# Optimization experiments

Hardware: AMD Instinct MI355X
Metric: run time of the kernel (lower is better)

The kernel has to match this reference:

```python
import jax, jax.numpy as jnp
import numpy as np

N_NODES = 50000
N_EDGES = 800000
IN_FEAT = 256
OUT_FEAT = 256
NUM_RELS = 8
ALPHA = 0.5


def setup_inputs() -> dict:
    key = jax.random.key(0)
    k1, k2, k3, k4, k5, k6 = jax.random.split(key, 6)
    x = jax.random.normal(k1, (N_NODES, IN_FEAT), dtype=jnp.float32)
    edge_index = jax.random.randint(k2, (2, N_EDGES), 0, N_NODES, dtype=jnp.int64)
    edge_type = jax.random.randint(k3, (N_EDGES,), 0, NUM_RELS, dtype=jnp.int64)
    # Xavier-uniform-ish init for weights (scale per fan-in/fan-out)
    gain = float(np.sqrt(2.0))  # calculate_gain('relu')
    lim_w = gain * float(np.sqrt(6.0 / (IN_FEAT + OUT_FEAT)))
    weight = jax.random.uniform(k4, (NUM_RELS, IN_FEAT, OUT_FEAT), dtype=jnp.float32,
                                minval=-lim_w, maxval=lim_w)
    loop_weight = jax.random.uniform(k5, (IN_FEAT, OUT_FEAT), dtype=jnp.float32,
                                     minval=-lim_w, maxval=lim_w)
    h_bias = jnp.zeros((OUT_FEAT,), dtype=jnp.float32)
    return {"edge_index": edge_index, "x": x, "edge_type": edge_type,
            "weight": weight, "h_bias": h_bias, "loop_weight": loop_weight}


def reference(edge_index, x, edge_type, weight, h_bias, loop_weight):
    num_nodes = x.shape[0]
    src, dst = edge_index[0], edge_index[1]
    # Per-edge message msg_e = x[src_e] @ weight[edge_type_e].
    # Computed efficiently as num_rels dense GEMMs over all nodes, then a fused
    # (relation, src) gather — identical math, avoids (E, in, out) weight blowup.
    hx = jnp.einsum('ni,rio->rno', x, weight)          # (R, N, out)
    msg = hx[edge_type, src]                            # (E, out)
    agg = jax.ops.segment_sum(msg, dst, num_segments=num_nodes)  # (N, out)
    node_repr = agg * jnp.asarray(ALPHA, x.dtype) ** 0.5
    node_repr = node_repr + h_bias
    loop_message = x @ loop_weight                      # (N, out)
    node_repr = node_repr + loop_message * jnp.asarray(1.0 - ALPHA, x.dtype) ** 0.5
    # activation=None, dropout=0.0 (eval) -> identity
    return node_repr
```

## Files before the change

### kernel.cpp

```cpp
#include <hip/hip_runtime.h>

typedef __bf16 bf16x8 __attribute__((ext_vector_type(8)));
typedef float f32x4 __attribute__((ext_vector_type(4)));

static __device__ __forceinline__ unsigned short f2bf(float f) {
    unsigned u = __builtin_bit_cast(unsigned, f);
    u += 0x7FFFu + ((u >> 16) & 1u);
    return (unsigned short)(u >> 16);
}
static __device__ __forceinline__ float bf2f(unsigned short h) {
    return __builtin_bit_cast(float, ((unsigned)h) << 16);
}

#define GLOAD_LDS16(g, l)                                              \
    __builtin_amdgcn_global_load_lds(                                  \
        (const __attribute__((address_space(1))) unsigned int*)(g),    \
        (__attribute__((address_space(3))) unsigned int*)(l), 16, 0, 0)

__global__ __launch_bounds__(256) void rgcn_zero(unsigned* __restrict__ p, int n) {
    int i = blockIdx.x * 256 + threadIdx.x;
    if (i < n) p[i] = 0;
}

__global__ __launch_bounds__(256) void rgcn_hist(const int* __restrict__ ei,
                                                 unsigned* __restrict__ cnt, int E) {
    int e = blockIdx.x * 256 + threadIdx.x;
    if (e < E) atomicAdd(&cnt[ei[E + e]], 1u);
}

__global__ __launch_bounds__(1024) void rgcn_scan1(const unsigned* __restrict__ cnt,
                                                   unsigned* __restrict__ off,
                                                   unsigned* __restrict__ bsum, int n) {
    __shared__ unsigned ws[16];
    const int t = threadIdx.x, lane = t & 63, wv = t >> 6;
    int i = blockIdx.x * 1024 + t;
    unsigned v = (i < n) ? cnt[i] : 0;
    unsigned s = v;
    #pragma unroll
    for (int d = 1; d < 64; d <<= 1) {
        unsigned u = __shfl_up(s, d, 64);
        if (lane >= d) s += u;
    }
    if (lane == 63) ws[wv] = s;
    __syncthreads();
    if (wv == 0) {
        unsigned b = (lane < 16) ? ws[lane] : 0;
        unsigned sb = b;
        #pragma unroll
        for (int d = 1; d < 16; d <<= 1) {
            unsigned u = __shfl_up(sb, d, 64);
            if (lane >= d) sb += u;
        }
        if (lane < 16) ws[lane] = sb - b;
        if (lane == 15) bsum[blockIdx.x] = sb;
    }
    __syncthreads();
    if (i < n) off[i] = ws[wv] + (s - v);
}

__global__ __launch_bounds__(64) void rgcn_scan2(unsigned* __restrict__ bsum,
                                                 unsigned* __restrict__ bsumo,
                                                 unsigned* __restrict__ off, int nb, int n) {
    const int lane = threadIdx.x & 63;
    unsigned b = (lane < nb) ? bsum[lane] : 0;
    unsigned s = b;
    #pragma unroll
    for (int d = 1; d < 64; d <<= 1) {
        unsigned u = __shfl_up(s, d, 64);
        if (lane >= d) s += u;
    }
    if (lane < nb) bsumo[lane] = s - b;
    if (lane == 63) off[n] = s;
}

__global__ __launch_bounds__(256) void rgcn_scan3(unsigned* __restrict__ off,
                                                  const unsigned* __restrict__ bsumo,
                                                  unsigned* __restrict__ cur, int n) {
    int i = blockIdx.x * 256 + threadIdx.x;
    if (i < n) {
        unsigned v = off[i] + bsumo[i >> 10];
        off[i] = v;
        cur[i] = v;
    }
}

__global__ __launch_bounds__(256) void rgcn_scatter(const int* __restrict__ ei,
                                                    const int* __restrict__ et,
                                                    unsigned* __restrict__ cur,
                                                    unsigned* __restrict__ recs, int E) {
    int e = blockIdx.x * 256 + threadIdx.x;
    if (e < E) {
        int dst = ei[E + e];
        unsigned p = atomicAdd(&cur[dst], 1u);
        recs[p] = (unsigned)ei[e] | ((unsigned)et[e] << 16);
    }
}

__global__ __launch_bounds__(256) void rgcn_cvt(const float* __restrict__ x,
                                                unsigned short* __restrict__ Z, int M) {
    int w = (blockIdx.x * 256 + threadIdx.x) >> 6;
    int lane = threadIdx.x & 63;
    if (w >= M) return;
    float4 v = *(const float4*)(x + (size_t)w * 256 + lane * 4);
    ushort4 o;
    o.x = f2bf(v.x); o.y = f2bf(v.y); o.z = f2bf(v.z); o.w = f2bf(v.w);
    *(ushort4*)(Z + (size_t)w * 2304 + 2048 + lane * 4) = o;
}

__global__ __launch_bounds__(256) void rgcn_wbt(const float* __restrict__ w,
                                                const float* __restrict__ lw,
                                                unsigned short* __restrict__ wbT) {
    int kc = blockIdx.x * 256 + threadIdx.x;
    int n  = blockIdx.y;
    if (kc >= 2304) return;
    float v;
    if (kc < 2048) {
        int r = kc >> 8, k = kc & 255;
        v = w[((size_t)r * 256 + k) * 256 + n];
    } else {
        v = lw[(size_t)(kc - 2048) * 256 + n];
    }
    wbT[(size_t)n * 2304 + kc] = f2bf(v * 0.70710678118654752f);
}

__global__ __launch_bounds__(256) void rgcn_agg(const unsigned* __restrict__ recs,
                                                const unsigned* __restrict__ off,
                                                unsigned short* __restrict__ Z, int M) {
    int w = (blockIdx.x * 256 + threadIdx.x) >> 6;
    int lane = threadIdx.x & 63;
    if (w >= M) return;
    unsigned o0 = off[w], o1 = off[w + 1];
    f32x4 a0 = {}, a1 = {}, a2 = {}, a3 = {}, a4 = {}, a5 = {}, a6 = {}, a7 = {};

#define LOADF(rec, fv)                                                                 \
    {                                                                                  \
        const ushort4 v_ = *(const ushort4*)(Z + (size_t)((rec) & 0xFFFFu) * 2304 +    \
                                             2048 + lane * 4);                         \
        fv[0] = bf2f(v_.x); fv[1] = bf2f(v_.y); fv[2] = bf2f(v_.z); fv[3] = bf2f(v_.w);\
    }
#define ACCUM(rec, fv)                                                                 \
    switch ((rec) >> 16) {                                                             \
        case 0: a0 += fv; break; case 1: a1 += fv; break;                              \
        case 2: a2 += fv; break; case 3: a3 += fv; break;                              \
        case 4: a4 += fv; break; case 5: a5 += fv; break;                              \
        case 6: a6 += fv; break; default: a7 += fv; break;                             \
    }

    unsigned i = o0;
    for (; i + 4 <= o1; i += 4) {
        unsigned r0 = recs[i], r1 = recs[i + 1], r2 = recs[i + 2], r3 = recs[i + 3];
        f32x4 f0, f1, f2, f3;
        LOADF(r0, f0); LOADF(r1, f1); LOADF(r2, f2); LOADF(r3, f3);
        ACCUM(r0, f0); ACCUM(r1, f1); ACCUM(r2, f2); ACCUM(r3, f3);
    }
    for (; i < o1; ++i) {
        unsigned r0 = recs[i];
        f32x4 f0;
        LOADF(r0, f0);
        ACCUM(r0, f0);
    }
#undef LOADF
#undef ACCUM

    unsigned short* zr = Z + (size_t)w * 2304 + lane * 4;
#define ST(rr, ax)                                                                     \
    {                                                                                  \
        ushort4 o_;                                                                    \
        o_.x = f2bf(ax[0]); o_.y = f2bf(ax[1]); o_.z = f2bf(ax[2]); o_.w = f2bf(ax[3]);\
        *(ushort4*)(zr + rr * 256) = o_;                                               \
    }
    ST(0, a0) ST(1, a1) ST(2, a2) ST(3, a3) ST(4, a4) ST(5, a5) ST(6, a6) ST(7, a7)
#undef ST
}

#define BM 128
#define BN 128
#define BK 64

__global__ __launch_bounds__(256) void rgcn_gemm(
    const unsigned short* __restrict__ A,
    const unsigned short* __restrict__ Bt,
    float* __restrict__ out,
    const float* __restrict__ bias,
    int M)
{
    __shared__ char lds[2 * BM * BK * 2];
    char* Ab = lds;
    char* Bb = lds + BM * BK * 2;

    const int tid  = threadIdx.x;
    const int lane = tid & 63;
    const int wid  = tid >> 6;
    const int wm   = (wid >> 1) * 64;
    const int wn   = (wid & 1) * 64;
    const int n0   = blockIdx.x * BN;
    const int m0   = blockIdx.y * BM;

    f32x4 acc[4][4] = {};

    int st_r[4], st_scb[4];
    #pragma unroll
    for (int it = 0; it < 4; ++it) {
        int o = it * 4096 + tid * 16;
        int r = o >> 7;
        st_r[it]   = r;
        st_scb[it] = (o & 127) ^ ((r & 7) << 4);
    }

    for (int kt = 0; kt < 2304; kt += BK) {
        __syncthreads();
        #pragma unroll
        for (int it = 0; it < 4; ++it) {
            const int r = st_r[it], scb = st_scb[it];
            int ga = m0 + r; if (ga >= M) ga = M - 1;
            const char* gA = (const char*)A + (size_t)ga * 4608 + (size_t)kt * 2 + scb;
            GLOAD_LDS16(gA, Ab + it * 4096 + tid * 16);
            const char* gB = (const char*)Bt + (size_t)(n0 + r) * 4608 + (size_t)kt * 2 + scb;
            GLOAD_LDS16(gB, Bb + it * 4096 + tid * 16);
        }
        __syncthreads();
        #pragma unroll
        for (int kk = 0; kk < 2; ++kk) {
            const int koff = kk * 32 + (lane >> 4) * 8;
            bf16x8 af[4], bfr[4];
            #pragma unroll
            for (int i = 0; i < 4; ++i) {
                int ar = wm + i * 16 + (lane & 15);
                af[i] = *(const bf16x8*)(Ab + ((ar * (BK * 2) + koff * 2) ^ ((ar & 7) << 4)));
                int br = wn + i * 16 + (lane & 15);
                bfr[i] = *(const bf16x8*)(Bb + ((br * (BK * 2) + koff * 2) ^ ((br & 7) << 4)));
            }
            #pragma unroll
            for (int i = 0; i < 4; ++i)
                #pragma unroll
                for (int j = 0; j < 4; ++j)
                    acc[i][j] = __builtin_amdgcn_mfma_f32_16x16x32_bf16(af[i], bfr[j], acc[i][j], 0, 0, 0);
        }
    }

    const int col = lane & 15;
    const int r0  = (lane >> 4) * 4;
    #pragma unroll
    for (int i = 0; i < 4; ++i) {
        #pragma unroll
        for (int j = 0; j < 4; ++j) {
            int gn = n0 + wn + j * 16 + col;
            float bv = bias[gn];
            #pragma unroll
            for (int rr = 0; rr < 4; ++rr) {
                int gm = m0 + wm + i * 16 + r0 + rr;
                if (gm < M) out[(size_t)gm * 256 + gn] = acc[i][j][rr] + bv;
            }
        }
    }
}

extern "C" void kernel_launch(void* const* d_in, const int* in_sizes, int n_in,
                              void* d_out, int out_size, void* d_ws, size_t ws_size,
                              hipStream_t stream) {
    const int*   edge_index = (const int*)d_in[0];
    const float* x          = (const float*)d_in[1];
    const int*   edge_type  = (const int*)d_in[2];
    const float* weight     = (const float*)d_in[3];
    const float* h_bias     = (const float*)d_in[4];
    const float* loop_w     = (const float*)d_in[5];
    float* out = (float*)d_out;

    const int M = in_sizes[1] / 256;
    const int E = in_sizes[2];

    char* ws = (char*)d_ws;
    size_t off_b = 0;
    unsigned short* Zcat = (unsigned short*)(ws + off_b);
    off_b += (((size_t)M * 2304 * 2) + 255) & ~(size_t)255;
    unsigned short* wbT = (unsigned short*)(ws + off_b);
    off_b += (((size_t)256 * 2304 * 2) + 255) & ~(size_t)255;
    unsigned* cnt = (unsigned*)(ws + off_b);
    off_b += (((size_t)(M + 1) * 4) + 255) & ~(size_t)255;
    unsigned* off = (unsigned*)(ws + off_b);
    off_b += (((size_t)(M + 1) * 4) + 255) & ~(size_t)255;
    unsigned* bsum = (unsigned*)(ws + off_b);
    off_b += 256;
    unsigned* bsumo = (unsigned*)(ws + off_b);
    off_b += 256;
    unsigned* recs = (unsigned*)(ws + off_b);

    const int nb = (M + 1023) / 1024;

    rgcn_zero<<<(M + 255) / 256, 256, 0, stream>>>(cnt, M);
    rgcn_hist<<<(E + 255) / 256, 256, 0, stream>>>(edge_index, cnt, E);
    rgcn_scan1<<<nb, 1024, 0, stream>>>(cnt, off, bsum, M);
    rgcn_scan2<<<1, 64, 0, stream>>>(bsum, bsumo, off, nb, M);
    rgcn_scan3<<<(M + 255) / 256, 256, 0, stream>>>(off, bsumo, cnt, M);
    rgcn_scatter<<<(E + 255) / 256, 256, 0, stream>>>(edge_index, edge_type, cnt, recs, E);

    rgcn_cvt<<<(M + 3) / 4, 256, 0, stream>>>(x, Zcat, M);
    rgcn_wbt<<<dim3(9, 256), 256, 0, stream>>>(weight, loop_w, wbT);

    rgcn_agg<<<(M + 3) / 4, 256, 0, stream>>>(recs, off, Zcat, M);

    rgcn_gemm<<<dim3(2, (M + BM - 1) / BM), 256, 0, stream>>>(Zcat, wbT, out, h_bias, M);
}
```

Before: 338.3 us.

## Widen GEMM tile to full output width and deepen aggregation unroll

The GEMM now has each block compute all 256 output columns for its 128-row tile (128x256 tile, 4x8 MFMA accumulators per wave). The large A operand (concatenated Z, K=2304) is therefore read from global memory once instead of twice across the two column blocks. The aggregation loop is unrolled to 8 edges to keep more gathers in flight, and its bf16 output is written with packed nontemporal 64-bit stores. The cost is more accumulator registers and larger LDS per block (48KB), which lowers occupancy, and only half as many GEMM blocks (~391) to spread across the CUs.

```diff
diff --git a/kernel.cpp b/kernel.cpp
--- a/kernel.cpp
+++ b/kernel.cpp
@@ -147,11 +147,14 @@
     }
 
     unsigned i = o0;
-    for (; i + 4 <= o1; i += 4) {
-        unsigned r0 = recs[i], r1 = recs[i + 1], r2 = recs[i + 2], r3 = recs[i + 3];
-        f32x4 f0, f1, f2, f3;
+    for (; i + 8 <= o1; i += 8) {
+        unsigned r0 = recs[i],     r1 = recs[i + 1], r2 = recs[i + 2], r3 = recs[i + 3];
+        unsigned r4 = recs[i + 4], r5 = recs[i + 5], r6 = recs[i + 6], r7 = recs[i + 7];
+        f32x4 f0, f1, f2, f3, f4, f5, f6, f7;
         LOADF(r0, f0); LOADF(r1, f1); LOADF(r2, f2); LOADF(r3, f3);
+        LOADF(r4, f4); LOADF(r5, f5); LOADF(r6, f6); LOADF(r7, f7);
         ACCUM(r0, f0); ACCUM(r1, f1); ACCUM(r2, f2); ACCUM(r3, f3);
+        ACCUM(r4, f4); ACCUM(r5, f5); ACCUM(r6, f6); ACCUM(r7, f7);
     }
     for (; i < o1; ++i) {
         unsigned r0 = recs[i];
@@ -165,16 +168,17 @@
     unsigned short* zr = Z + (size_t)w * 2304 + lane * 4;
 #define ST(rr, ax)                                                                     \
     {                                                                                  \
-        ushort4 o_;                                                                    \
-        o_.x = f2bf(ax[0]); o_.y = f2bf(ax[1]); o_.z = f2bf(ax[2]); o_.w = f2bf(ax[3]);\
-        *(ushort4*)(zr + rr * 256) = o_;                                               \
+        unsigned lo_ = (unsigned)f2bf(ax[0]) | ((unsigned)f2bf(ax[1]) << 16);          \
+        unsigned hi_ = (unsigned)f2bf(ax[2]) | ((unsigned)f2bf(ax[3]) << 16);          \
+        unsigned long long v_ = (unsigned long long)lo_ |                              \
+                                ((unsigned long long)hi_ << 32);                       \
+        __builtin_nontemporal_store(v_, (unsigned long long*)(zr + rr * 256));         \
     }
     ST(0, a0) ST(1, a1) ST(2, a2) ST(3, a3) ST(4, a4) ST(5, a5) ST(6, a6) ST(7, a7)
 #undef ST
 }
 
 #define BM 128
-#define BN 128
 #define BK 64
 
 __global__ __launch_bounds__(256) void rgcn_gemm(
@@ -184,56 +188,55 @@
     const float* __restrict__ bias,
     int M)
 {
-    __shared__ char lds[2 * BM * BK * 2];
+    __shared__ char lds[16384 + 32768];
     char* Ab = lds;
-    char* Bb = lds + BM * BK * 2;
+    char* Bb = lds + 16384;
 
     const int tid  = threadIdx.x;
     const int lane = tid & 63;
     const int wid  = tid >> 6;
     const int wm   = (wid >> 1) * 64;
-    const int wn   = (wid & 1) * 64;
-    const int n0   = blockIdx.x * BN;
-    const int m0   = blockIdx.y * BM;
-
-    f32x4 acc[4][4] = {};
-
-    int st_r[4], st_scb[4];
-    #pragma unroll
-    for (int it = 0; it < 4; ++it) {
-        int o = it * 4096 + tid * 16;
-        int r = o >> 7;
-        st_r[it]   = r;
-        st_scb[it] = (o & 127) ^ ((r & 7) << 4);
-    }
+    const int wn   = (wid & 1) * 128;
+    const int m0   = blockIdx.x * BM;
+
+    f32x4 acc[4][8] = {};
 
     for (int kt = 0; kt < 2304; kt += BK) {
         __syncthreads();
         #pragma unroll
         for (int it = 0; it < 4; ++it) {
-            const int r = st_r[it], scb = st_scb[it];
-            int ga = m0 + r; if (ga >= M) ga = M - 1;
-            const char* gA = (const char*)A + (size_t)ga * 4608 + (size_t)kt * 2 + scb;
-            GLOAD_LDS16(gA, Ab + it * 4096 + tid * 16);
-            const char* gB = (const char*)Bt + (size_t)(n0 + r) * 4608 + (size_t)kt * 2 + scb;
-            GLOAD_LDS16(gB, Bb + it * 4096 + tid * 16);
+            int o   = it * 4096 + tid * 16;
+            int r   = o >> 7;
+            int scb = (o & 127) ^ ((r & 7) << 4);
+            int ga  = m0 + r; if (ga >= M) ga = M - 1;
+            GLOAD_LDS16((const char*)A + (size_t)ga * 4608 + (size_t)kt * 2 + scb, Ab + o);
+        }
+        #pragma unroll
+        for (int it = 0; it < 8; ++it) {
+            int o   = it * 4096 + tid * 16;
+            int r   = o >> 7;
+            int scb = (o & 127) ^ ((r & 7) << 4);
+            GLOAD_LDS16((const char*)Bt + (size_t)r * 4608 + (size_t)kt * 2 + scb, Bb + o);
         }
         __syncthreads();
         #pragma unroll
         for (int kk = 0; kk < 2; ++kk) {
             const int koff = kk * 32 + (lane >> 4) * 8;
-            bf16x8 af[4], bfr[4];
+            bf16x8 af[4], bfr[8];
             #pragma unroll
             for (int i = 0; i < 4; ++i) {
                 int ar = wm + i * 16 + (lane & 15);
-                af[i] = *(const bf16x8*)(Ab + ((ar * (BK * 2) + koff * 2) ^ ((ar & 7) << 4)));
-                int br = wn + i * 16 + (lane & 15);
-                bfr[i] = *(const bf16x8*)(Bb + ((br * (BK * 2) + koff * 2) ^ ((br & 7) << 4)));
+                af[i] = *(const bf16x8*)(Ab + ((ar * 128 + koff * 2) ^ ((ar & 7) << 4)));
+            }
+            #pragma unroll
+            for (int j = 0; j < 8; ++j) {
+                int br = wn + j * 16 + (lane & 15);
+                bfr[j] = *(const bf16x8*)(Bb + ((br * 128 + koff * 2) ^ ((br & 7) << 4)));
             }
             #pragma unroll
             for (int i = 0; i < 4; ++i)
                 #pragma unroll
-                for (int j = 0; j < 4; ++j)
+                for (int j = 0; j < 8; ++j)
                     acc[i][j] = __builtin_amdgcn_mfma_f32_16x16x32_bf16(af[i], bfr[j], acc[i][j], 0, 0, 0);
         }
     }
@@ -243,8 +246,8 @@
     #pragma unroll
     for (int i = 0; i < 4; ++i) {
         #pragma unroll
-        for (int j = 0; j < 4; ++j) {
-            int gn = n0 + wn + j * 16 + col;
+        for (int j = 0; j < 8; ++j) {
+            int gn = wn + j * 16 + col;
             float bv = bias[gn];
             #pragma unroll
             for (int rr = 0; rr < 4; ++rr) {
@@ -299,5 +302,5 @@
 
     rgcn_agg<<<(M + 3) / 4, 256, 0, stream>>>(recs, off, Zcat, M);
 
-    rgcn_gemm<<<dim3(2, (M + BM - 1) / BM), 256, 0, stream>>>(Zcat, wbT, out, h_bias, M);
-}
+    rgcn_gemm<<<(M + BM - 1) / BM, 256, 0, stream>>>(Zcat, wbT, out, h_bias, M);
+}
```

New measurement: 390.6 us. 15.4% more time.
